# Kernel tuning notes

Measured on AMD Instinct MI355X. Metric: run time of the kernel, lower is better.

The kernel has to match this reference:

```python
import jax, jax.numpy as jnp
import numpy as np

B, S, D = 4, 2048, 1024
H = 16
DK = D // H  # 64


def setup_inputs() -> dict:
    key = jax.random.key(0)
    k1, k2, k3 = jax.random.split(key, 3)
    std_qkv = (2.0 / (D + 3 * D)) ** 0.5
    std_o = (2.0 / (D + D)) ** 0.5
    x = jax.random.normal(k1, (B, S, D), dtype=jnp.float32)
    W_qkv = jax.random.normal(k2, (3 * D, D), dtype=jnp.float32) * std_qkv
    W_o = jax.random.normal(k3, (D, D), dtype=jnp.float32) * std_o
    return {"x": x, "W_qkv": W_qkv, "W_o": W_o}


def reference(x, W_qkv, W_o):
    b, s, d = x.shape
    # qkv projection: [b, s, 3*H*DK]
    qkv = jnp.einsum('bsd,ed->bse', x, W_qkv)
    # rearrange '(c h dk)' -> c, b, h, s, dk
    qkv = qkv.reshape(b, s, 3, H, DK)
    qkv = jnp.transpose(qkv, (2, 0, 3, 1, 4))  # [3, b, h, s, dk]
    q, k, v = qkv[0], qkv[1], qkv[2]
    # scaled dot product attention with causal mask
    scores = jnp.einsum('bhqd,bhkd->bhqk', q, k) / (DK ** 0.5)
    causal = jnp.tril(jnp.ones((s, s), dtype=bool))
    scores = jnp.where(causal, scores, -jnp.inf)
    probs = jax.nn.softmax(scores, axis=-1)
    heads = jnp.einsum('bhqk,bhkd->bhqd', probs, v)
    # merge heads: [b, s, H*DK]
    heads = jnp.transpose(heads, (0, 2, 1, 3)).reshape(b, s, H * DK)
    return jnp.einsum('bse,de->bsd', heads, W_o)
```

## Files before the change

kernel.cpp:

```cpp
#include <hip/hip_runtime.h>
#include <hip/hip_bf16.h>

#define BB 4
#define SS 2048
#define DD 1024
#define HH 16
#define DKK 64

typedef __bf16 bf16x8 __attribute__((ext_vector_type(8)));
typedef float floatx4 __attribute__((ext_vector_type(4)));

#if __has_builtin(__builtin_amdgcn_exp2f)
#define EXP2(x) __builtin_amdgcn_exp2f(x)
#else
#define EXP2(x) exp2f(x)
#endif

__device__ __forceinline__ float b2f(unsigned short u) {
    union { unsigned int i; float f; } c;
    c.i = ((unsigned int)u) << 16;
    return c.f;
}
__device__ __forceinline__ unsigned short f2b(float f) {
    unsigned int i = __float_as_uint(f);
    unsigned int r = (i + 0x7FFFu + ((i >> 16) & 1u)) >> 16;
    return (unsigned short)r;
}
__device__ __forceinline__ unsigned int pkpair(float a, float b) {
    unsigned int ia = (__float_as_uint(a) + 0x8000u) >> 16;
    unsigned int ib = (__float_as_uint(b) + 0x8000u) & 0xffff0000u;
    return ia | ib;
}

__device__ __forceinline__ void gload_lds16(const unsigned short* g,
                                            unsigned short* l) {
    __builtin_amdgcn_global_load_lds(
        (const __attribute__((address_space(1))) unsigned int*)g,
        (__attribute__((address_space(3))) unsigned int*)l, 16, 0, 0);
}

__global__ void cvt_f32_bf16(const float* __restrict__ in,
                             unsigned short* __restrict__ out, int n4) {
    int i = blockIdx.x * blockDim.x + threadIdx.x;
    if (i >= n4) return;
    float4 v = ((const float4*)in)[i];
    ushort4 o;
    o.x = f2b(v.x); o.y = f2b(v.y); o.z = f2b(v.z); o.w = f2b(v.w);
    ((ushort4*)out)[i] = o;
}

template <typename CT>
__global__ __launch_bounds__(512, 2) void gemm_nt_8ph(
    const unsigned short* __restrict__ A,
    const unsigned short* __restrict__ B,
    CT* __restrict__ C, int M, int N, int K) {
    extern __shared__ unsigned short lds[];
    unsigned short* At = lds;
    unsigned short* Bt = lds + 2 * 256 * 64;

    const int tid  = threadIdx.x;
    const int lane = tid & 63;
    const int w    = tid >> 6;
    const int wm   = (w >> 1) * 64;
    const int wn   = (w & 1) * 64;

    const int m0 = blockIdx.x * 256;
    const int n0 = blockIdx.y * 128;

    const int row16 = lane & 15;
    const int part  = lane >> 4;
    const int rbase = part * 4;

    const int srow  = lane >> 3;
    const int scol  = ((lane & 7) * 8) ^ ((srow & 6) << 2);

    const unsigned short* Ag = A + (size_t)(m0 + srow) * K + scol;
    const unsigned short* Bg = B + (size_t)(n0 + srow) * K + scol;

    const int NT = K >> 6;
    floatx4 acc[4][4] = {};

    const int shr = (row16 & 6) << 2;

#define STAGE(t, bb)                                                        \
    {                                                                       \
        const size_t koff = (size_t)(t) * 64;                               \
        _Pragma("unroll") for (int a = 0; a < 4; ++a) {                     \
            const int rb = (w * 4 + a) * 8;                                 \
            gload_lds16(Ag + (size_t)rb * K + koff,                         \
                        At + (bb) * 16384 + rb * 64);                       \
        }                                                                   \
        _Pragma("unroll") for (int bi = 0; bi < 2; ++bi) {                  \
            const int rb = (w * 2 + bi) * 8;                                \
            gload_lds16(Bg + (size_t)rb * K + koff,                         \
                        Bt + (bb) * 8192 + rb * 64);                        \
        }                                                                   \
    }

    STAGE(0, 0);

    for (int t = 0; t < NT; ++t) {
        const int cur = t & 1;
        if (t + 1 < NT) {
            STAGE(t + 1, cur ^ 1);
            asm volatile("s_waitcnt vmcnt(6)" ::: "memory");
        } else {
            asm volatile("s_waitcnt vmcnt(0)" ::: "memory");
        }
        __builtin_amdgcn_sched_barrier(0);
        __builtin_amdgcn_s_barrier();

        const unsigned short* Ab = At + cur * 16384;
        const unsigned short* Bb = Bt + cur * 8192;

        bf16x8 bf[4][2];
#pragma unroll
        for (int j = 0; j < 4; ++j)
#pragma unroll
            for (int u = 0; u < 2; ++u)
                bf[j][u] = *(const bf16x8*)(Bb + (wn + j * 16 + row16) * 64 +
                                            ((u * 32 + part * 8) ^ shr));

#pragma unroll
        for (int qm = 0; qm < 2; ++qm) {
            bf16x8 af[2][2];
#pragma unroll
            for (int i = 0; i < 2; ++i)
#pragma unroll
                for (int u = 0; u < 2; ++u)
                    af[i][u] = *(const bf16x8*)(
                        Ab + (wm + (qm * 2 + i) * 16 + row16) * 64 +
                        ((u * 32 + part * 8) ^ shr));
#pragma unroll
            for (int qn = 0; qn < 2; ++qn) {
                __builtin_amdgcn_s_barrier();
                asm volatile("s_waitcnt lgkmcnt(0)" ::: "memory");
                __builtin_amdgcn_sched_barrier(0);
                __builtin_amdgcn_s_setprio(1);
#pragma unroll
                for (int i = 0; i < 2; ++i)
#pragma unroll
                    for (int j = 0; j < 2; ++j)
#pragma unroll
                        for (int u = 0; u < 2; ++u)
                            acc[qm * 2 + i][qn * 2 + j] =
                                __builtin_amdgcn_mfma_f32_16x16x32_bf16(
                                    af[i][u], bf[qn * 2 + j][u],
                                    acc[qm * 2 + i][qn * 2 + j], 0, 0, 0);
                __builtin_amdgcn_s_setprio(0);
                __builtin_amdgcn_sched_barrier(0);
                __builtin_amdgcn_s_barrier();
            }
        }
    }
#undef STAGE

#pragma unroll
    for (int i = 0; i < 4; ++i) {
#pragma unroll
        for (int j = 0; j < 4; ++j) {
            const int row = m0 + wm + i * 16 + rbase;
            const int col = n0 + wn + j * 16 + row16;
#pragma unroll
            for (int r = 0; r < 4; ++r) {
                size_t idx = (size_t)(row + r) * N + col;
                if constexpr (sizeof(CT) == 2) C[idx] = f2b(acc[i][j][r]);
                else                           C[idx] = acc[i][j][r];
            }
        }
    }
}

__global__ void repack_kv(const unsigned short* __restrict__ qkv,
                          unsigned short* __restrict__ Kp,
                          unsigned short* __restrict__ Vt) {
    __shared__ unsigned short Vs[64][72];
    const int st = blockIdx.x, h = blockIdx.y, b = blockIdx.z;
    const int tid = threadIdx.x;
    const size_t base = ((size_t)((b * HH + h) * (SS / 64) + st)) * 4096;

#pragma unroll
    for (int p = 0; p < 2; ++p) {
        const int row = p * 32 + (tid >> 3);
        const int chunk = tid & 7;
        size_t src = (size_t)(b * SS + st * 64 + row) * (3 * DD) +
                     DD + h * DKK + chunk * 8;
        uint4 kv = *(const uint4*)(qkv + src);
        *(uint4*)(Kp + base + (chunk >> 2) * 2048 + row * 32 + (chunk & 3) * 8) = kv;
        uint4 vv = *(const uint4*)(qkv + src + DD);
        *(uint4*)&Vs[row][chunk * 8] = vv;
    }
    __syncthreads();
#pragma unroll
    for (int p = 0; p < 2; ++p) {
        const int dk = p * 32 + (tid >> 3);
        const int s8 = tid & 7;
        union { unsigned short u[8]; uint4 v; } pk;
#pragma unroll
        for (int j = 0; j < 8; ++j) pk.u[j] = Vs[s8 * 8 + j][dk];
        *(uint4*)(Vt + base + (s8 >> 2) * 2048 + dk * 32 + (s8 & 3) * 8) = pk.v;
    }
}

struct StripState {
    bf16x8 qf[2][2];
    floatx4 O[2][4];
    float mrow[2], lrow[2];
    int q0w;
};

__device__ __forceinline__ void strip_init(
    StripState& S, const unsigned short* __restrict__ qkv,
    int b, int h, int q0w, int row16, int part) {
    const float c1 = 0.180336884f;
    S.q0w = q0w;
#pragma unroll
    for (int qt = 0; qt < 2; ++qt) {
        S.mrow[qt] = -1e30f;
        S.lrow[qt] = 0.f;
#pragma unroll
        for (int dt = 0; dt < 4; ++dt) S.O[qt][dt] = floatx4{0, 0, 0, 0};
#pragma unroll
        for (int u = 0; u < 2; ++u) {
            const unsigned short* qp = qkv +
                (size_t)(b * SS + q0w + qt * 16 + row16) * (3 * DD) +
                h * DKK + u * 32 + part * 8;
            union { uint4 r; unsigned short us[8]; } raw;
            raw.r = *(const uint4*)qp;
            union { unsigned short us[8]; bf16x8 v; } sq;
#pragma unroll
            for (int j = 0; j < 8; ++j) sq.us[j] = f2b(b2f(raw.us[j]) * c1);
            S.qf[qt][u] = sq.v;
        }
    }
}

__device__ __forceinline__ void strip_tile(
    StripState& S, int k0, const bf16x8 kf[2][4], const bf16x8 vf[2][4],
    int row16, int part, int rbase) {
#pragma unroll
    for (int qt = 0; qt < 2; ++qt) {
        floatx4 sc[4] = {};
#pragma unroll
        for (int u = 0; u < 2; ++u)
#pragma unroll
            for (int kt = 0; kt < 4; ++kt)
                sc[kt] = __builtin_amdgcn_mfma_f32_16x16x32_bf16(
                    kf[u][kt], S.qf[qt][u], sc[kt], 0, 0, 0);

        const int qa = S.q0w + qt * 16 + row16;
        const bool full = (k0 + 63 <= S.q0w + qt * 16);
        float mx = -1e30f;
#pragma unroll
        for (int kt = 0; kt < 4; ++kt)
#pragma unroll
            for (int r = 0; r < 4; ++r) {
                float s = sc[kt][r];
                if (!full) {
                    int ka = k0 + kt * 16 + rbase + r;
                    s = (ka <= qa) ? s : -1e30f;
                }
                sc[kt][r] = s;
                mx = fmaxf(mx, s);
            }
        mx = fmaxf(mx, __shfl_xor(mx, 16));
        mx = fmaxf(mx, __shfl_xor(mx, 32));
        float mnew = fmaxf(S.mrow[qt], mx);
        float alpha = EXP2(S.mrow[qt] - mnew);

        float ps = 0.f;
        unsigned int pk[4][2];
#pragma unroll
        for (int kt = 0; kt < 4; ++kt) {
            float e0 = EXP2(sc[kt][0] - mnew);
            float e1 = EXP2(sc[kt][1] - mnew);
            float e2 = EXP2(sc[kt][2] - mnew);
            float e3 = EXP2(sc[kt][3] - mnew);
            ps += (e0 + e1) + (e2 + e3);
            pk[kt][0] = pkpair(e0, e1);
            pk[kt][1] = pkpair(e2, e3);
        }
        ps += __shfl_xor(ps, 16);
        ps += __shfl_xor(ps, 32);
        S.lrow[qt] = S.lrow[qt] * alpha + ps;
        S.mrow[qt] = mnew;

#pragma unroll
        for (int dt = 0; dt < 4; ++dt) S.O[qt][dt] *= alpha;

        const int l0 = row16 + ((part & 1) * 2 + 0) * 16;
        const int l1 = row16 + ((part & 1) * 2 + 1) * 16;
        const bool hi = (part >> 1);
#pragma unroll
        for (int u = 0; u < 2; ++u) {
            unsigned int lo00 = (unsigned int)__shfl((int)pk[2 * u][0], l0);
            unsigned int lo01 = (unsigned int)__shfl((int)pk[2 * u][1], l0);
            unsigned int lo10 = (unsigned int)__shfl((int)pk[2 * u][0], l1);
            unsigned int lo11 = (unsigned int)__shfl((int)pk[2 * u][1], l1);
            unsigned int hi00 = (unsigned int)__shfl((int)pk[2 * u + 1][0], l0);
            unsigned int hi01 = (unsigned int)__shfl((int)pk[2 * u + 1][1], l0);
            unsigned int hi10 = (unsigned int)__shfl((int)pk[2 * u + 1][0], l1);
            unsigned int hi11 = (unsigned int)__shfl((int)pk[2 * u + 1][1], l1);
            union { unsigned int u32[4]; bf16x8 v; } P;
            P.u32[0] = hi ? hi00 : lo00;
            P.u32[1] = hi ? hi01 : lo01;
            P.u32[2] = hi ? hi10 : lo10;
            P.u32[3] = hi ? hi11 : lo11;
#pragma unroll
            for (int dt = 0; dt < 4; ++dt)
                S.O[qt][dt] = __builtin_amdgcn_mfma_f32_16x16x32_bf16(
                    vf[u][dt], P.v, S.O[qt][dt], 0, 0, 0);
        }
    }
}

__device__ __forceinline__ void strip_store(
    StripState& S, unsigned short* __restrict__ heads,
    int b, int h, int row16, int rbase) {
#pragma unroll
    for (int qt = 0; qt < 2; ++qt) {
        float inv = 1.f / S.lrow[qt];
#pragma unroll
        for (int dt = 0; dt < 4; ++dt) {
            ushort4 o4;
            o4.x = f2b(S.O[qt][dt][0] * inv);
            o4.y = f2b(S.O[qt][dt][1] * inv);
            o4.z = f2b(S.O[qt][dt][2] * inv);
            o4.w = f2b(S.O[qt][dt][3] * inv);
            size_t base = (size_t)(b * SS + S.q0w + qt * 16 + row16) * DD +
                          h * DKK + dt * 16 + rbase;
            *(ushort4*)&heads[base] = o4;
        }
    }
}

__global__ __launch_bounds__(256, 2) void attn_mfma6(
    const unsigned short* __restrict__ qkv,
    const unsigned short* __restrict__ Kp,
    const unsigned short* __restrict__ Vt,
    unsigned short* __restrict__ heads) {
    const int tid  = threadIdx.x;
    const int lane = tid & 63;
    const int w    = tid >> 6;

    const int bx   = blockIdx.x;
    const int xcd  = bx & 7;
    const int slot = bx >> 3;
    const int pair = xcd * 8 + (slot >> 3);
    const int blk  = slot & 7;
    const int b = pair >> 4, h = pair & 15;

    const int jA = blk * 4 + w;
    const int jB = 63 - jA;
    const int ntA = jA / 2 + 1;
    const int ntB = jB / 2 + 1;

    const int row16 = lane & 15;
    const int part  = lane >> 4;
    const int rbase = part * 4;

    StripState SA, SB;
    strip_init(SA, qkv, b, h, jA * 32, row16, part);
    strip_init(SB, qkv, b, h, jB * 32, row16, part);

    const size_t tb = (size_t)pair * (SS / 64) * 4096;

    for (int t = 0; t < ntB; ++t) {
        const int k0 = t * 64;
        const unsigned short* kbase = Kp + tb + (size_t)t * 4096;
        const unsigned short* vbase = Vt + tb + (size_t)t * 4096;
        bf16x8 kf[2][4], vf[2][4];
#pragma unroll
        for (int u = 0; u < 2; ++u)
#pragma unroll
            for (int i = 0; i < 4; ++i) {
                kf[u][i] = *(const bf16x8*)(kbase + u * 2048 +
                                            (i * 16 + row16) * 32 + part * 8);
                vf[u][i] = *(const bf16x8*)(vbase + u * 2048 +
                                            (i * 16 + row16) * 32 + part * 8);
            }
        strip_tile(SB, k0, kf, vf, row16, part, rbase);
        if (t < ntA) strip_tile(SA, k0, kf, vf, row16, part, rbase);
    }

    strip_store(SA, heads, b, h, row16, rbase);
    strip_store(SB, heads, b, h, row16, rbase);
}

extern "C" void kernel_launch(void* const* d_in, const int* in_sizes, int n_in,
                              void* d_out, int out_size, void* d_ws,
                              size_t ws_size, hipStream_t stream) {
    const float* x    = (const float*)d_in[0];
    const float* Wqkv = (const float*)d_in[1];
    const float* Wo   = (const float*)d_in[2];
    float* out = (float*)d_out;

    const size_t NX  = (size_t)BB * SS * DD;
    const size_t NWQ = (size_t)3 * DD * DD;
    const size_t NWO = (size_t)DD * DD;
    const size_t NKV = (size_t)BB * HH * SS * DKK;

    unsigned short* xb     = (unsigned short*)d_ws;
    unsigned short* wqkvb  = xb + NX;
    unsigned short* wob    = wqkvb + NWQ;
    unsigned short* qkvb   = wob + NWO;
    unsigned short* headsb = qkvb + (size_t)BB * SS * 3 * DD;
    unsigned short* Kp     = headsb + NX;
    unsigned short* Vtp    = Kp + NKV;

    static bool attr_done = false;
    if (!attr_done) {
        hipFuncSetAttribute(
            reinterpret_cast<const void*>(&gemm_nt_8ph<unsigned short>),
            hipFuncAttributeMaxDynamicSharedMemorySize, 98304);
        hipFuncSetAttribute(
            reinterpret_cast<const void*>(&gemm_nt_8ph<float>),
            hipFuncAttributeMaxDynamicSharedMemorySize, 98304);
        attr_done = true;
    }

    cvt_f32_bf16<<<(int)(NX / 4 / 256), 256, 0, stream>>>(x, xb, (int)(NX / 4));
    cvt_f32_bf16<<<(int)(NWQ / 4 / 256), 256, 0, stream>>>(Wqkv, wqkvb, (int)(NWQ / 4));
    cvt_f32_bf16<<<(int)(NWO / 4 / 256), 256, 0, stream>>>(Wo, wob, (int)(NWO / 4));

    gemm_nt_8ph<unsigned short><<<dim3(BB * SS / 256, 3 * DD / 128), 512,
                                  98304, stream>>>(xb, wqkvb, qkvb,
                                                   BB * SS, 3 * DD, DD);

    repack_kv<<<dim3(SS / 64, HH, BB), 256, 0, stream>>>(qkvb, Kp, Vtp);

    attn_mfma6<<<dim3(512), 256, 0, stream>>>(qkvb, Kp, Vtp, headsb);

    gemm_nt_8ph<float><<<dim3(BB * SS / 256, DD / 128), 512, 98304, stream>>>(
        headsb, wob, out, BB * SS, DD, DD);
}
```

Baseline: 277.6 us.

## Triple-buffer GEMM LDS pipeline and skip small online-softmax rescales

The projection GEMMs move from double- to triple-buffered LDS staging with a new swizzle and load layout, issuing the load for tile t+2 after the barrier and cutting the inner phases from four barrier-separated groups to two. This aims to hide global-load latency better, at the cost of 144 KB of LDS per block, which probably limits residency to one block per CU on a 160 KB LDS. The attention kernel adds a lazy-rescale rule: the running max and the O accumulator are only updated when some lane's new max exceeds the old by more than 8 in log2 units. This removes exp and multiply work in the common case, but lets the exponentials grow up to 2^8, which bounds bf16 and fp32 accuracy risk.

```diff
diff --git a/kernel.cpp b/kernel.cpp
--- a/kernel.cpp
+++ b/kernel.cpp
@@ -50,13 +50,11 @@
 }
 
 template <typename CT>
-__global__ __launch_bounds__(512, 2) void gemm_nt_8ph(
+__global__ __launch_bounds__(512, 2) void gemm_nt_3buf(
     const unsigned short* __restrict__ A,
     const unsigned short* __restrict__ B,
     CT* __restrict__ C, int M, int N, int K) {
     extern __shared__ unsigned short lds[];
-    unsigned short* At = lds;
-    unsigned short* Bt = lds + 2 * 256 * 64;
 
     const int tid  = threadIdx.x;
     const int lane = tid & 63;
@@ -71,38 +69,35 @@
     const int part  = lane >> 4;
     const int rbase = part * 4;
 
-    const int srow  = lane >> 3;
-    const int scol  = ((lane & 7) * 8) ^ ((srow & 6) << 2);
-
+    const int srow = tid >> 3;
+    const int scol = ((tid & 7) * 8) ^ ((srow & 7) << 3);
     const unsigned short* Ag = A + (size_t)(m0 + srow) * K + scol;
     const unsigned short* Bg = B + (size_t)(n0 + srow) * K + scol;
 
     const int NT = K >> 6;
     floatx4 acc[4][4] = {};
 
-    const int shr = (row16 & 6) << 2;
-
-#define STAGE(t, bb)                                                        \
+    const int shr = (row16 & 7) << 3;
+
+#define STAGE3(t, bb)                                                       \
     {                                                                       \
         const size_t koff = (size_t)(t) * 64;                               \
-        _Pragma("unroll") for (int a = 0; a < 4; ++a) {                     \
-            const int rb = (w * 4 + a) * 8;                                 \
-            gload_lds16(Ag + (size_t)rb * K + koff,                         \
-                        At + (bb) * 16384 + rb * 64);                       \
-        }                                                                   \
-        _Pragma("unroll") for (int bi = 0; bi < 2; ++bi) {                  \
-            const int rb = (w * 2 + bi) * 8;                                \
-            gload_lds16(Bg + (size_t)rb * K + koff,                         \
-                        Bt + (bb) * 8192 + rb * 64);                        \
-        }                                                                   \
-    }
-
-    STAGE(0, 0);
-
+        unsigned short* Abuf = lds + (bb) * 24576;                          \
+        unsigned short* Bbuf = Abuf + 16384;                                \
+        _Pragma("unroll") for (int r = 0; r < 4; ++r)                       \
+            gload_lds16(Ag + (size_t)(r * 64) * K + koff,                   \
+                        Abuf + r * 4096 + w * 512);                         \
+        _Pragma("unroll") for (int r = 0; r < 2; ++r)                       \
+            gload_lds16(Bg + (size_t)(r * 64) * K + koff,                   \
+                        Bbuf + r * 4096 + w * 512);                         \
+    }
+
+    STAGE3(0, 0);
+    STAGE3(1, 1);
+
+    int cur = 0;
     for (int t = 0; t < NT; ++t) {
-        const int cur = t & 1;
         if (t + 1 < NT) {
-            STAGE(t + 1, cur ^ 1);
             asm volatile("s_waitcnt vmcnt(6)" ::: "memory");
         } else {
             asm volatile("s_waitcnt vmcnt(0)" ::: "memory");
@@ -110,50 +105,72 @@
         __builtin_amdgcn_sched_barrier(0);
         __builtin_amdgcn_s_barrier();
 
-        const unsigned short* Ab = At + cur * 16384;
-        const unsigned short* Bb = Bt + cur * 8192;
-
-        bf16x8 bf[4][2];
+        if (t + 2 < NT) {
+            int nb = cur + 2;
+            if (nb >= 3) nb -= 3;
+            STAGE3(t + 2, nb);
+        }
+
+        const unsigned short* Ab = lds + cur * 24576;
+        const unsigned short* Bb = Ab + 16384;
+
+        bf16x8 bf[4][2], af[2][2];
 #pragma unroll
         for (int j = 0; j < 4; ++j)
 #pragma unroll
             for (int u = 0; u < 2; ++u)
                 bf[j][u] = *(const bf16x8*)(Bb + (wn + j * 16 + row16) * 64 +
                                             ((u * 32 + part * 8) ^ shr));
-
-#pragma unroll
-        for (int qm = 0; qm < 2; ++qm) {
-            bf16x8 af[2][2];
-#pragma unroll
-            for (int i = 0; i < 2; ++i)
+#pragma unroll
+        for (int i = 0; i < 2; ++i)
+#pragma unroll
+            for (int u = 0; u < 2; ++u)
+                af[i][u] = *(const bf16x8*)(Ab + (wm + i * 16 + row16) * 64 +
+                                            ((u * 32 + part * 8) ^ shr));
+
+        __builtin_amdgcn_s_barrier();
+        asm volatile("s_waitcnt lgkmcnt(0)" ::: "memory");
+        __builtin_amdgcn_sched_barrier(0);
+        __builtin_amdgcn_s_setprio(1);
+#pragma unroll
+        for (int i = 0; i < 2; ++i)
+#pragma unroll
+            for (int j = 0; j < 4; ++j)
 #pragma unroll
                 for (int u = 0; u < 2; ++u)
-                    af[i][u] = *(const bf16x8*)(
-                        Ab + (wm + (qm * 2 + i) * 16 + row16) * 64 +
-                        ((u * 32 + part * 8) ^ shr));
-#pragma unroll
-            for (int qn = 0; qn < 2; ++qn) {
-                __builtin_amdgcn_s_barrier();
-                asm volatile("s_waitcnt lgkmcnt(0)" ::: "memory");
-                __builtin_amdgcn_sched_barrier(0);
-                __builtin_amdgcn_s_setprio(1);
-#pragma unroll
-                for (int i = 0; i < 2; ++i)
-#pragma unroll
-                    for (int j = 0; j < 2; ++j)
-#pragma unroll
-                        for (int u = 0; u < 2; ++u)
-                            acc[qm * 2 + i][qn * 2 + j] =
-                                __builtin_amdgcn_mfma_f32_16x16x32_bf16(
-                                    af[i][u], bf[qn * 2 + j][u],
-                                    acc[qm * 2 + i][qn * 2 + j], 0, 0, 0);
-                __builtin_amdgcn_s_setprio(0);
-                __builtin_amdgcn_sched_barrier(0);
-                __builtin_amdgcn_s_barrier();
-            }
-        }
-    }
-#undef STAGE
+                    acc[i][j] = __builtin_amdgcn_mfma_f32_16x16x32_bf16(
+                        af[i][u], bf[j][u], acc[i][j], 0, 0, 0);
+        __builtin_amdgcn_s_setprio(0);
+        __builtin_amdgcn_sched_barrier(0);
+        __builtin_amdgcn_s_barrier();
+
+#pragma unroll
+        for (int i = 0; i < 2; ++i)
+#pragma unroll
+            for (int u = 0; u < 2; ++u)
+                af[i][u] = *(const bf16x8*)(
+                    Ab + (wm + (2 + i) * 16 + row16) * 64 +
+                    ((u * 32 + part * 8) ^ shr));
+
+        __builtin_amdgcn_s_barrier();
+        asm volatile("s_waitcnt lgkmcnt(0)" ::: "memory");
+        __builtin_amdgcn_sched_barrier(0);
+        __builtin_amdgcn_s_setprio(1);
+#pragma unroll
+        for (int i = 0; i < 2; ++i)
+#pragma unroll
+            for (int j = 0; j < 4; ++j)
+#pragma unroll
+                for (int u = 0; u < 2; ++u)
+                    acc[2 + i][j] = __builtin_amdgcn_mfma_f32_16x16x32_bf16(
+                        af[i][u], bf[j][u], acc[2 + i][j], 0, 0, 0);
+        __builtin_amdgcn_s_setprio(0);
+        __builtin_amdgcn_sched_barrier(0);
+
+        ++cur;
+        if (cur >= 3) cur -= 3;
+    }
+#undef STAGE3
 
 #pragma unroll
     for (int i = 0; i < 4; ++i) {
@@ -265,8 +282,9 @@
             }
         mx = fmaxf(mx, __shfl_xor(mx, 16));
         mx = fmaxf(mx, __shfl_xor(mx, 32));
-        float mnew = fmaxf(S.mrow[qt], mx);
-        float alpha = EXP2(S.mrow[qt] - mnew);
+
+        const bool resc = !__all(mx - S.mrow[qt] <= 8.f);
+        float mnew = resc ? fmaxf(S.mrow[qt], mx) : S.mrow[qt];
 
         float ps = 0.f;
         unsigned int pk[4][2];
@@ -282,11 +300,15 @@
         }
         ps += __shfl_xor(ps, 16);
         ps += __shfl_xor(ps, 32);
-        S.lrow[qt] = S.lrow[qt] * alpha + ps;
-        S.mrow[qt] = mnew;
-
-#pragma unroll
-        for (int dt = 0; dt < 4; ++dt) S.O[qt][dt] *= alpha;
+        if (resc) {
+            float alpha = EXP2(S.mrow[qt] - mnew);
+            S.lrow[qt] = S.lrow[qt] * alpha + ps;
+            S.mrow[qt] = mnew;
+#pragma unroll
+            for (int dt = 0; dt < 4; ++dt) S.O[qt][dt] *= alpha;
+        } else {
+            S.lrow[qt] += ps;
+        }
 
         const int l0 = row16 + ((part & 1) * 2 + 0) * 16;
         const int l1 = row16 + ((part & 1) * 2 + 1) * 16;
@@ -411,11 +433,11 @@
     static bool attr_done = false;
     if (!attr_done) {
         hipFuncSetAttribute(
-            reinterpret_cast<const void*>(&gemm_nt_8ph<unsigned short>),
-            hipFuncAttributeMaxDynamicSharedMemorySize, 98304);
+            reinterpret_cast<const void*>(&gemm_nt_3buf<unsigned short>),
+            hipFuncAttributeMaxDynamicSharedMemorySize, 147456);
         hipFuncSetAttribute(
-            reinterpret_cast<const void*>(&gemm_nt_8ph<float>),
-            hipFuncAttributeMaxDynamicSharedMemorySize, 98304);
+            reinterpret_cast<const void*>(&gemm_nt_3buf<float>),
+            hipFuncAttributeMaxDynamicSharedMemorySize, 147456);
         attr_done = true;
     }
 
@@ -423,14 +445,14 @@
     cvt_f32_bf16<<<(int)(NWQ / 4 / 256), 256, 0, stream>>>(Wqkv, wqkvb, (int)(NWQ / 4));
     cvt_f32_bf16<<<(int)(NWO / 4 / 256), 256, 0, stream>>>(Wo, wob, (int)(NWO / 4));
 
-    gemm_nt_8ph<unsigned short><<<dim3(BB * SS / 256, 3 * DD / 128), 512,
-                                  98304, stream>>>(xb, wqkvb, qkvb,
-                                                   BB * SS, 3 * DD, DD);
+    gemm_nt_3buf<unsigned short><<<dim3(BB * SS / 256, 3 * DD / 128), 512,
+                                   147456, stream>>>(xb, wqkvb, qkvb,
+                                                     BB * SS, 3 * DD, DD);
 
     repack_kv<<<dim3(SS / 64, HH, BB), 256, 0, stream>>>(qkvb, Kp, Vtp);
 
     attn_mfma6<<<dim3(512), 256, 0, stream>>>(qkvb, Kp, Vtp, headsb);
 
-    gemm_nt_8ph<float><<<dim3(BB * SS / 256, DD / 128), 512, 98304, stream>>>(
+    gemm_nt_3buf<float><<<dim3(BB * SS / 256, DD / 128), 512, 147456, stream>>>(
         headsb, wob, out, BB * SS, DD, DD);
 }
```

Result: faster. 262.2 us (-5.6%).

## Enlarge GEMM tiles to 256x256 and add lazy softmax rescaling in attention

Applied to the files above, without the earlier changes.

The projection GEMM switches from 256x128 to 256x256 block tiles, with each wave computing a 128x64 sub-tile and a new 8-row XOR swizzle. This raises arithmetic intensity per LDS byte but uses 128KB of LDS, so only one block fits per CU, and the output GEMM grid drops to 128 blocks. Separately, the attention kernel skips the online-softmax rescale of O and l unless the wave-wide max grows by more than 8 in log2 units, saving exp and multiply work per tile.

```diff
diff --git a/kernel.cpp b/kernel.cpp
--- a/kernel.cpp
+++ b/kernel.cpp
@@ -50,117 +50,107 @@
 }
 
 template <typename CT>
-__global__ __launch_bounds__(512, 2) void gemm_nt_8ph(
+__global__ __launch_bounds__(512, 2) void gemm_nt_256(
     const unsigned short* __restrict__ A,
     const unsigned short* __restrict__ B,
     CT* __restrict__ C, int M, int N, int K) {
     extern __shared__ unsigned short lds[];
-    unsigned short* At = lds;
-    unsigned short* Bt = lds + 2 * 256 * 64;
 
     const int tid  = threadIdx.x;
     const int lane = tid & 63;
     const int w    = tid >> 6;
-    const int wm   = (w >> 1) * 64;
-    const int wn   = (w & 1) * 64;
+    const int wmh  = w >> 2;
+    const int wnq  = w & 3;
 
     const int m0 = blockIdx.x * 256;
-    const int n0 = blockIdx.y * 128;
+    const int n0 = blockIdx.y * 256;
 
     const int row16 = lane & 15;
     const int part  = lane >> 4;
     const int rbase = part * 4;
-
-    const int srow  = lane >> 3;
-    const int scol  = ((lane & 7) * 8) ^ ((srow & 6) << 2);
-
+    const int shr   = (row16 & 7) << 3;
+
+    const int srow = tid >> 3;
+    const int scol = ((tid & 7) * 8) ^ ((srow & 7) << 3);
     const unsigned short* Ag = A + (size_t)(m0 + srow) * K + scol;
     const unsigned short* Bg = B + (size_t)(n0 + srow) * K + scol;
+    const int ldsw = w * 512;
 
     const int NT = K >> 6;
-    floatx4 acc[4][4] = {};
-
-    const int shr = (row16 & 6) << 2;
-
-#define STAGE(t, bb)                                                        \
-    {                                                                       \
-        const size_t koff = (size_t)(t) * 64;                               \
-        _Pragma("unroll") for (int a = 0; a < 4; ++a) {                     \
-            const int rb = (w * 4 + a) * 8;                                 \
-            gload_lds16(Ag + (size_t)rb * K + koff,                         \
-                        At + (bb) * 16384 + rb * 64);                       \
-        }                                                                   \
-        _Pragma("unroll") for (int bi = 0; bi < 2; ++bi) {                  \
-            const int rb = (w * 2 + bi) * 8;                                \
-            gload_lds16(Bg + (size_t)rb * K + koff,                         \
-                        Bt + (bb) * 8192 + rb * 64);                        \
-        }                                                                   \
-    }
-
-    STAGE(0, 0);
-
-    for (int t = 0; t < NT; ++t) {
-        const int cur = t & 1;
-        if (t + 1 < NT) {
-            STAGE(t + 1, cur ^ 1);
-            asm volatile("s_waitcnt vmcnt(6)" ::: "memory");
-        } else {
-            asm volatile("s_waitcnt vmcnt(0)" ::: "memory");
-        }
-        __builtin_amdgcn_sched_barrier(0);
-        __builtin_amdgcn_s_barrier();
-
-        const unsigned short* Ab = At + cur * 16384;
-        const unsigned short* Bb = Bt + cur * 8192;
-
-        bf16x8 bf[4][2];
-#pragma unroll
-        for (int j = 0; j < 4; ++j)
-#pragma unroll
-            for (int u = 0; u < 2; ++u)
-                bf[j][u] = *(const bf16x8*)(Bb + (wn + j * 16 + row16) * 64 +
-                                            ((u * 32 + part * 8) ^ shr));
-
-#pragma unroll
-        for (int qm = 0; qm < 2; ++qm) {
+    floatx4 acc[8][4] = {};
+
+#define STAGE_TILE(t)                                                    \
+    {                                                                    \
+        unsigned short* sb = lds + ((t) & 1) * 32768;                    \
+        const size_t ko = (size_t)(t) * 64;                              \
+        _Pragma("unroll") for (int r2 = 0; r2 < 4; ++r2)                 \
+            gload_lds16(Ag + (size_t)(r2 * 64) * K + ko,                 \
+                        sb + r2 * 4096 + ldsw);                          \
+        _Pragma("unroll") for (int r2 = 0; r2 < 4; ++r2)                 \
+            gload_lds16(Bg + (size_t)(r2 * 64) * K + ko,                 \
+                        sb + 16384 + r2 * 4096 + ldsw);                  \
+    }
+
+    STAGE_TILE(0);
+
+    bf16x8 bfr[4][2];
+    for (int kt = 0; kt < NT; ++kt) {
+        const unsigned short* Ab = lds + (kt & 1) * 32768;
+        const unsigned short* Bb = Ab + 16384;
+#pragma unroll
+        for (int q = 0; q < 4; ++q) {
+            if (q == 0) {
+                if (kt + 1 < NT) {
+                    STAGE_TILE(kt + 1);
+                    asm volatile("s_waitcnt vmcnt(8)" ::: "memory");
+                } else {
+                    asm volatile("s_waitcnt vmcnt(0)" ::: "memory");
+                }
+                __builtin_amdgcn_sched_barrier(0);
+                __builtin_amdgcn_s_barrier();
+#pragma unroll
+                for (int j = 0; j < 4; ++j)
+#pragma unroll
+                    for (int u = 0; u < 2; ++u)
+                        bfr[j][u] = *(const bf16x8*)(
+                            Bb + (wnq * 64 + j * 16 + row16) * 64 +
+                            ((u * 32 + part * 8) ^ shr));
+            }
             bf16x8 af[2][2];
 #pragma unroll
             for (int i = 0; i < 2; ++i)
 #pragma unroll
                 for (int u = 0; u < 2; ++u)
                     af[i][u] = *(const bf16x8*)(
-                        Ab + (wm + (qm * 2 + i) * 16 + row16) * 64 +
+                        Ab + (wmh * 128 + (q * 2 + i) * 16 + row16) * 64 +
                         ((u * 32 + part * 8) ^ shr));
-#pragma unroll
-            for (int qn = 0; qn < 2; ++qn) {
-                __builtin_amdgcn_s_barrier();
-                asm volatile("s_waitcnt lgkmcnt(0)" ::: "memory");
-                __builtin_amdgcn_sched_barrier(0);
-                __builtin_amdgcn_s_setprio(1);
-#pragma unroll
-                for (int i = 0; i < 2; ++i)
-#pragma unroll
-                    for (int j = 0; j < 2; ++j)
-#pragma unroll
-                        for (int u = 0; u < 2; ++u)
-                            acc[qm * 2 + i][qn * 2 + j] =
-                                __builtin_amdgcn_mfma_f32_16x16x32_bf16(
-                                    af[i][u], bf[qn * 2 + j][u],
-                                    acc[qm * 2 + i][qn * 2 + j], 0, 0, 0);
-                __builtin_amdgcn_s_setprio(0);
-                __builtin_amdgcn_sched_barrier(0);
-                __builtin_amdgcn_s_barrier();
-            }
-        }
-    }
-#undef STAGE
-
-#pragma unroll
-    for (int i = 0; i < 4; ++i) {
+            __builtin_amdgcn_s_barrier();
+            asm volatile("s_waitcnt lgkmcnt(0)" ::: "memory");
+            __builtin_amdgcn_sched_barrier(0);
+            __builtin_amdgcn_s_setprio(1);
+#pragma unroll
+            for (int i = 0; i < 2; ++i)
+#pragma unroll
+                for (int j = 0; j < 4; ++j)
+#pragma unroll
+                    for (int u = 0; u < 2; ++u)
+                        acc[q * 2 + i][j] =
+                            __builtin_amdgcn_mfma_f32_16x16x32_bf16(
+                                af[i][u], bfr[j][u], acc[q * 2 + i][j],
+                                0, 0, 0);
+            __builtin_amdgcn_s_setprio(0);
+            __builtin_amdgcn_sched_barrier(0);
+            __builtin_amdgcn_s_barrier();
+        }
+    }
+#undef STAGE_TILE
+
+#pragma unroll
+    for (int i = 0; i < 8; ++i) {
 #pragma unroll
         for (int j = 0; j < 4; ++j) {
-            const int row = m0 + wm + i * 16 + rbase;
-            const int col = n0 + wn + j * 16 + row16;
+            const int row = m0 + wmh * 128 + i * 16 + rbase;
+            const int col = n0 + wnq * 64 + j * 16 + row16;
 #pragma unroll
             for (int r = 0; r < 4; ++r) {
                 size_t idx = (size_t)(row + r) * N + col;
@@ -265,8 +255,9 @@
             }
         mx = fmaxf(mx, __shfl_xor(mx, 16));
         mx = fmaxf(mx, __shfl_xor(mx, 32));
-        float mnew = fmaxf(S.mrow[qt], mx);
-        float alpha = EXP2(S.mrow[qt] - mnew);
+
+        const bool resc = !__all(mx - S.mrow[qt] <= 8.f);
+        float mnew = resc ? fmaxf(S.mrow[qt], mx) : S.mrow[qt];
 
         float ps = 0.f;
         unsigned int pk[4][2];
@@ -282,11 +273,15 @@
         }
         ps += __shfl_xor(ps, 16);
         ps += __shfl_xor(ps, 32);
-        S.lrow[qt] = S.lrow[qt] * alpha + ps;
-        S.mrow[qt] = mnew;
-
-#pragma unroll
-        for (int dt = 0; dt < 4; ++dt) S.O[qt][dt] *= alpha;
+        if (resc) {
+            float alpha = EXP2(S.mrow[qt] - mnew);
+            S.lrow[qt] = S.lrow[qt] * alpha + ps;
+            S.mrow[qt] = mnew;
+#pragma unroll
+            for (int dt = 0; dt < 4; ++dt) S.O[qt][dt] *= alpha;
+        } else {
+            S.lrow[qt] += ps;
+        }
 
         const int l0 = row16 + ((part & 1) * 2 + 0) * 16;
         const int l1 = row16 + ((part & 1) * 2 + 1) * 16;
@@ -411,11 +406,11 @@
     static bool attr_done = false;
     if (!attr_done) {
         hipFuncSetAttribute(
-            reinterpret_cast<const void*>(&gemm_nt_8ph<unsigned short>),
-            hipFuncAttributeMaxDynamicSharedMemorySize, 98304);
+            reinterpret_cast<const void*>(&gemm_nt_256<unsigned short>),
+            hipFuncAttributeMaxDynamicSharedMemorySize, 131072);
         hipFuncSetAttribute(
-            reinterpret_cast<const void*>(&gemm_nt_8ph<float>),
-            hipFuncAttributeMaxDynamicSharedMemorySize, 98304);
+            reinterpret_cast<const void*>(&gemm_nt_256<float>),
+            hipFuncAttributeMaxDynamicSharedMemorySize, 131072);
         attr_done = true;
     }
 
@@ -423,14 +418,14 @@
     cvt_f32_bf16<<<(int)(NWQ / 4 / 256), 256, 0, stream>>>(Wqkv, wqkvb, (int)(NWQ / 4));
     cvt_f32_bf16<<<(int)(NWO / 4 / 256), 256, 0, stream>>>(Wo, wob, (int)(NWO / 4));
 
-    gemm_nt_8ph<unsigned short><<<dim3(BB * SS / 256, 3 * DD / 128), 512,
-                                  98304, stream>>>(xb, wqkvb, qkvb,
-                                                   BB * SS, 3 * DD, DD);
+    gemm_nt_256<unsigned short><<<dim3(BB * SS / 256, 3 * DD / 256), 512,
+                                  131072, stream>>>(xb, wqkvb, qkvb,
+                                                    BB * SS, 3 * DD, DD);
 
     repack_kv<<<dim3(SS / 64, HH, BB), 256, 0, stream>>>(qkvb, Kp, Vtp);
 
     attn_mfma6<<<dim3(512), 256, 0, stream>>>(qkvb, Kp, Vtp, headsb);
 
-    gemm_nt_8ph<float><<<dim3(BB * SS / 256, DD / 128), 512, 98304, stream>>>(
+    gemm_nt_256<float><<<dim3(BB * SS / 256, DD / 256), 512, 131072, stream>>>(
         headsb, wob, out, BB * SS, DD, DD);
 }
```

Measured after the change: 283.7 us. 2.2% more time.
